# Optimization experiments

Hardware: AMD Instinct MI355X
Metric: run time of the kernel (lower is better)

The kernel has to match this reference:

```python
import jax, jax.numpy as jnp
import numpy as np

B, H, N = 1024, 1024, 32  # batch, d_model, d_state//2 (conjugate-symmetric diag)

def setup_inputs() -> dict:
    key = jax.random.key(0)
    ks = jax.random.split(key, 12)
    return {
        "u": jax.random.normal(ks[0], (B, H), jnp.float32),
        "state_re": jax.random.normal(ks[1], (B, H, N), jnp.float32),
        "state_im": jax.random.normal(ks[2], (B, H, N), jnp.float32),
        "dA_re": jax.random.normal(ks[3], (H, N), jnp.float32) * 0.3,
        "dA_im": jax.random.normal(ks[4], (H, N), jnp.float32) * 0.3,
        "dB_re": jax.random.normal(ks[5], (H, N), jnp.float32),
        "dB_im": jax.random.normal(ks[6], (H, N), jnp.float32),
        "C_re": jax.random.normal(ks[7], (H, N), jnp.float32),
        "C_im": jax.random.normal(ks[8], (H, N), jnp.float32),
        "D": jax.random.normal(ks[9], (H,), jnp.float32),
        "W": jax.random.normal(ks[10], (2 * H, H), jnp.float32) / np.sqrt(H),
        "b": jax.random.normal(ks[11], (2 * H,), jnp.float32) * 0.01,
    }

def reference(u, state_re, state_im, dA_re, dA_im, dB_re, dB_im, C_re, C_im, D, W, b):
    # Complex diagonal state update: next_state = dA * state + dB * u   [B,H,N]
    ue = u[..., None]
    ns_re = dA_re * state_re - dA_im * state_im + dB_re * ue
    ns_im = dA_re * state_im + dA_im * state_re + dB_im * ue
    # Readout: y = 2 * Re(sum_n C * next_state)   [B,H]  (channels=1)
    y = 2.0 * (jnp.einsum('hn,bhn->bh', C_re, ns_re)
               - jnp.einsum('hn,bhn->bh', C_im, ns_im))
    # Skip connection + exact GELU (torch default)
    y = jax.nn.gelu(y + u * D, approximate=False)
    # output_linear: Linear(H -> 2H) then GLU
    z = y @ W.T + b                      # [B, 2H]
    h = D.shape[0]
    y_out = z[:, :h] * jax.nn.sigmoid(z[:, h:])
    return y_out, ns_re, ns_im
```

## Files before the change

kernel.cpp:

```cpp
#include <hip/hip_runtime.h>
#include <math.h>

#define BB 1024
#define HH 1024
#define NN 32

typedef float f4 __attribute__((ext_vector_type(4)));

__global__ __launch_bounds__(256) void s4_update_kernel(
    const float* __restrict__ u,
    const float* __restrict__ sre,  const float* __restrict__ sim,
    const float* __restrict__ dAre, const float* __restrict__ dAim,
    const float* __restrict__ dBre, const float* __restrict__ dBim,
    const float* __restrict__ Cre,  const float* __restrict__ Cim,
    const float* __restrict__ Dv,
    float* __restrict__ nsre, float* __restrict__ nsim,
    float* __restrict__ Y)
{
    const int tid  = threadIdx.x;
    const long gid = (long)blockIdx.x * 256 + tid;
    const int pair = (int)(gid >> 3);
    const int sub  = tid & 7;
    const int n0   = sub << 2;
    const int h    = pair & (HH - 1);
    const size_t sbase = (size_t)pair * NN + n0;
    const int    pbase = h * NN + n0;

    const f4 a_re = *(const f4*)(dAre + pbase);
    const f4 a_im = *(const f4*)(dAim + pbase);
    const f4 b_re = *(const f4*)(dBre + pbase);
    const f4 b_im = *(const f4*)(dBim + pbase);
    const f4 c_re = *(const f4*)(Cre  + pbase);
    const f4 c_im = *(const f4*)(Cim  + pbase);
    const f4 s_re = *(const f4*)(sre + sbase);
    const f4 s_im = *(const f4*)(sim + sbase);
    const float uv = u[pair];

    f4 nre = a_re * s_re - a_im * s_im + b_re * uv;
    f4 nim = a_re * s_im + a_im * s_re + b_im * uv;

    *(f4*)(nsre + sbase) = nre;
    *(f4*)(nsim + sbase) = nim;

    f4 p = c_re * nre - c_im * nim;
    float part = p[0] + p[1] + p[2] + p[3];
    part += __shfl_xor(part, 1, 64);
    part += __shfl_xor(part, 2, 64);
    part += __shfl_xor(part, 4, 64);

    if (sub == 0) {
        float yv = 2.0f * part + uv * Dv[h];
        float g = 0.5f * yv * (1.0f + erff(yv * 0.70710678118654752f));
        Y[pair] = g;
    }
}

__global__ __launch_bounds__(256) void s4_gemm_glu_kernel(
    const float* __restrict__ Y, const float* __restrict__ W,
    const float* __restrict__ bias, float* __restrict__ out)
{
    __shared__ float Ys [16][68];
    __shared__ float W1s[16][68];
    __shared__ float W2s[16][68];

    const int tid  = threadIdx.x;
    const int row0 = blockIdx.y * 64;
    const int jc0  = blockIdx.x * 64;

    const int lr = tid >> 2;
    const int lk = (tid & 3) << 2;

    const float* Yg  = Y + (size_t)(row0 + lr) * HH + lk;
    const float* W1g = W + (size_t)(jc0 + lr) * HH + lk;
    const float* W2g = W + (size_t)(jc0 + 1024 + lr) * HH + lk;

    const int tc = tid & 15;
    const int tr = tid >> 4;

    float acc1[4][4] = {{0.f}};
    float acc2[4][4] = {{0.f}};

    for (int k0 = 0; k0 < HH; k0 += 16) {
        const f4 yv = *(const f4*)(Yg  + k0);
        const f4 w1 = *(const f4*)(W1g + k0);
        const f4 w2 = *(const f4*)(W2g + k0);

        __syncthreads();
        #pragma unroll
        for (int i = 0; i < 4; ++i) {
            Ys [lk + i][lr] = yv[i];
            W1s[lk + i][lr] = w1[i];
            W2s[lk + i][lr] = w2[i];
        }
        __syncthreads();

        #pragma unroll
        for (int kk = 0; kk < 16; ++kk) {
            const f4 ya  = *(const f4*)&Ys [kk][tr << 2];
            const f4 wa1 = *(const f4*)&W1s[kk][tc << 2];
            const f4 wa2 = *(const f4*)&W2s[kk][tc << 2];
            #pragma unroll
            for (int i = 0; i < 4; ++i) {
                #pragma unroll
                for (int j = 0; j < 4; ++j) {
                    acc1[i][j] = fmaf(ya[i], wa1[j], acc1[i][j]);
                    acc2[i][j] = fmaf(ya[i], wa2[j], acc2[i][j]);
                }
            }
        }
    }

    float b1[4], b2[4];
    #pragma unroll
    for (int j = 0; j < 4; ++j) {
        b1[j] = bias[jc0 + (tc << 2) + j];
        b2[j] = bias[jc0 + 1024 + (tc << 2) + j];
    }
    #pragma unroll
    for (int i = 0; i < 4; ++i) {
        f4 o;
        #pragma unroll
        for (int j = 0; j < 4; ++j) {
            float z1 = acc1[i][j] + b1[j];
            float z2 = acc2[i][j] + b2[j];
            o[j] = z1 * (1.0f / (1.0f + expf(-z2)));
        }
        *(f4*)(out + (size_t)(row0 + (tr << 2) + i) * HH + jc0 + (tc << 2)) = o;
    }
}

extern "C" void kernel_launch(void* const* d_in, const int* in_sizes, int n_in,
                              void* d_out, int out_size, void* d_ws, size_t ws_size,
                              hipStream_t stream) {
    const float* u    = (const float*)d_in[0];
    const float* sre  = (const float*)d_in[1];
    const float* sim  = (const float*)d_in[2];
    const float* dAre = (const float*)d_in[3];
    const float* dAim = (const float*)d_in[4];
    const float* dBre = (const float*)d_in[5];
    const float* dBim = (const float*)d_in[6];
    const float* Cre  = (const float*)d_in[7];
    const float* Cim  = (const float*)d_in[8];
    const float* Dv   = (const float*)d_in[9];
    const float* W    = (const float*)d_in[10];
    const float* bias = (const float*)d_in[11];

    float* out   = (float*)d_out;
    float* y_out = out;
    float* nsre  = out + (size_t)BB * HH;
    float* nsim  = nsre + (size_t)BB * HH * NN;
    float* Yws   = (float*)d_ws;

    const long total_threads = (long)BB * HH * 8;
    s4_update_kernel<<<dim3((unsigned)(total_threads / 256)), 256, 0, stream>>>(
        u, sre, sim, dAre, dAim, dBre, dBim, Cre, Cim, Dv, nsre, nsim, Yws);

    s4_gemm_glu_kernel<<<dim3(16, 16), 256, 0, stream>>>(Yws, W, bias, y_out);
}
```

Before: 565.8 us.

## Replace FP32 SIMT GEMM with split-bf16 MFMA GEMM fused with GLU

Splits Y and W into high and low bf16 parts (the update kernel writes Y's parts, a new kernel converts W each call). The GEMM becomes a matrix-core kernel that runs three bf16 MFMA products (hi*hi, hi*lo, lo*hi) to approximate FP32 accuracy, with GLU in the epilogue. It trades scalar FMA work for matrix-core throughput but adds a W conversion pass, extra workspace traffic and loads straight from global memory without LDS staging.

```diff
diff --git a/kernel.cpp b/kernel.cpp
--- a/kernel.cpp
+++ b/kernel.cpp
@@ -5,7 +5,20 @@
 #define HH 1024
 #define NN 32
 
-typedef float f4 __attribute__((ext_vector_type(4)));
+typedef float f4     __attribute__((ext_vector_type(4)));
+typedef float f32x4  __attribute__((ext_vector_type(4)));
+typedef short bf16x8 __attribute__((ext_vector_type(8)));
+typedef short s4v    __attribute__((ext_vector_type(4)));
+
+static __device__ __forceinline__ short f2bf(float x) {
+    unsigned u = __builtin_bit_cast(unsigned, x);
+    u += 0x7fff + ((u >> 16) & 1);
+    return (short)(u >> 16);
+}
+static __device__ __forceinline__ float bf2f(short h) {
+    unsigned u = ((unsigned)(unsigned short)h) << 16;
+    return __builtin_bit_cast(float, u);
+}
 
 __global__ __launch_bounds__(256) void s4_update_kernel(
     const float* __restrict__ u,
@@ -15,7 +28,7 @@
     const float* __restrict__ Cre,  const float* __restrict__ Cim,
     const float* __restrict__ Dv,
     float* __restrict__ nsre, float* __restrict__ nsim,
-    float* __restrict__ Y)
+    short* __restrict__ Yhi, short* __restrict__ Ylo)
 {
     const int tid  = threadIdx.x;
     const long gid = (long)blockIdx.x * 256 + tid;
@@ -51,81 +64,98 @@
     if (sub == 0) {
         float yv = 2.0f * part + uv * Dv[h];
         float g = 0.5f * yv * (1.0f + erff(yv * 0.70710678118654752f));
-        Y[pair] = g;
+        short hi = f2bf(g);
+        Yhi[pair] = hi;
+        Ylo[pair] = f2bf(g - bf2f(hi));
     }
 }
 
-__global__ __launch_bounds__(256) void s4_gemm_glu_kernel(
-    const float* __restrict__ Y, const float* __restrict__ W,
+__global__ __launch_bounds__(256) void wsplit_kernel(
+    const float* __restrict__ W, short* __restrict__ Whi, short* __restrict__ Wlo)
+{
+    const size_t i = ((size_t)blockIdx.x * 256 + threadIdx.x) * 4;
+    const f4 w = *(const f4*)(W + i);
+    s4v hi, lo;
+    #pragma unroll
+    for (int j = 0; j < 4; ++j) {
+        hi[j] = f2bf(w[j]);
+        lo[j] = f2bf(w[j] - bf2f(hi[j]));
+    }
+    *(s4v*)(Whi + i) = hi;
+    *(s4v*)(Wlo + i) = lo;
+}
+
+__global__ __launch_bounds__(256) void gemm_mfma_glu_kernel(
+    const short* __restrict__ Yhi, const short* __restrict__ Ylo,
+    const short* __restrict__ Whi, const short* __restrict__ Wlo,
     const float* __restrict__ bias, float* __restrict__ out)
 {
-    __shared__ float Ys [16][68];
-    __shared__ float W1s[16][68];
-    __shared__ float W2s[16][68];
+    const int tid  = threadIdx.x;
+    const int lane = tid & 63;
+    const int w    = tid >> 6;
+    const int wr   = w >> 1;
+    const int wc   = w & 1;
+    const int l15  = lane & 15;
+    const int g    = lane >> 4;
 
-    const int tid  = threadIdx.x;
-    const int row0 = blockIdx.y * 64;
-    const int jc0  = blockIdx.x * 64;
+    const int r0 = blockIdx.y * 64 + wr * 32;
+    const int jc = blockIdx.x * 32 + wc * 16;
 
-    const int lr = tid >> 2;
-    const int lk = (tid & 3) << 2;
+    const size_t rowA0 = (size_t)(r0 + l15) * HH;
+    const size_t rowA1 = rowA0 + (size_t)16 * HH;
+    const size_t rowB1 = (size_t)(jc + l15) * HH;
+    const size_t rowB2 = (size_t)(HH + jc + l15) * HH;
+    const int koff = g * 8;
 
-    const float* Yg  = Y + (size_t)(row0 + lr) * HH + lk;
-    const float* W1g = W + (size_t)(jc0 + lr) * HH + lk;
-    const float* W2g = W + (size_t)(jc0 + 1024 + lr) * HH + lk;
+    const short* pAh0 = Yhi + rowA0 + koff;
+    const short* pAh1 = Yhi + rowA1 + koff;
+    const short* pAl0 = Ylo + rowA0 + koff;
+    const short* pAl1 = Ylo + rowA1 + koff;
+    const short* pBh1 = Whi + rowB1 + koff;
+    const short* pBh2 = Whi + rowB2 + koff;
+    const short* pBl1 = Wlo + rowB1 + koff;
+    const short* pBl2 = Wlo + rowB2 + koff;
 
-    const int tc = tid & 15;
-    const int tr = tid >> 4;
+    f32x4 acc[2][2] = {};
 
-    float acc1[4][4] = {{0.f}};
-    float acc2[4][4] = {{0.f}};
+    #pragma unroll 2
+    for (int k0 = 0; k0 < HH; k0 += 32) {
+        const bf16x8 ah0 = *(const bf16x8*)(pAh0 + k0);
+        const bf16x8 ah1 = *(const bf16x8*)(pAh1 + k0);
+        const bf16x8 al0 = *(const bf16x8*)(pAl0 + k0);
+        const bf16x8 al1 = *(const bf16x8*)(pAl1 + k0);
+        const bf16x8 bh1 = *(const bf16x8*)(pBh1 + k0);
+        const bf16x8 bh2 = *(const bf16x8*)(pBh2 + k0);
+        const bf16x8 bl1 = *(const bf16x8*)(pBl1 + k0);
+        const bf16x8 bl2 = *(const bf16x8*)(pBl2 + k0);
 
-    for (int k0 = 0; k0 < HH; k0 += 16) {
-        const f4 yv = *(const f4*)(Yg  + k0);
-        const f4 w1 = *(const f4*)(W1g + k0);
-        const f4 w2 = *(const f4*)(W2g + k0);
+        acc[0][0] = __builtin_amdgcn_mfma_f32_16x16x32_bf16(ah0, bh1, acc[0][0], 0, 0, 0);
+        acc[0][1] = __builtin_amdgcn_mfma_f32_16x16x32_bf16(ah0, bh2, acc[0][1], 0, 0, 0);
+        acc[1][0] = __builtin_amdgcn_mfma_f32_16x16x32_bf16(ah1, bh1, acc[1][0], 0, 0, 0);
+        acc[1][1] = __builtin_amdgcn_mfma_f32_16x16x32_bf16(ah1, bh2, acc[1][1], 0, 0, 0);
 
-        __syncthreads();
-        #pragma unroll
-        for (int i = 0; i < 4; ++i) {
-            Ys [lk + i][lr] = yv[i];
-            W1s[lk + i][lr] = w1[i];
-            W2s[lk + i][lr] = w2[i];
-        }
-        __syncthreads();
+        acc[0][0] = __builtin_amdgcn_mfma_f32_16x16x32_bf16(ah0, bl1, acc[0][0], 0, 0, 0);
+        acc[0][1] = __builtin_amdgcn_mfma_f32_16x16x32_bf16(ah0, bl2, acc[0][1], 0, 0, 0);
+        acc[1][0] = __builtin_amdgcn_mfma_f32_16x16x32_bf16(ah1, bl1, acc[1][0], 0, 0, 0);
+        acc[1][1] = __builtin_amdgcn_mfma_f32_16x16x32_bf16(ah1, bl2, acc[1][1], 0, 0, 0);
 
-        #pragma unroll
-        for (int kk = 0; kk < 16; ++kk) {
-            const f4 ya  = *(const f4*)&Ys [kk][tr << 2];
-            const f4 wa1 = *(const f4*)&W1s[kk][tc << 2];
-            const f4 wa2 = *(const f4*)&W2s[kk][tc << 2];
-            #pragma unroll
-            for (int i = 0; i < 4; ++i) {
-                #pragma unroll
-                for (int j = 0; j < 4; ++j) {
-                    acc1[i][j] = fmaf(ya[i], wa1[j], acc1[i][j]);
-                    acc2[i][j] = fmaf(ya[i], wa2[j], acc2[i][j]);
-                }
-            }
-        }
+        acc[0][0] = __builtin_amdgcn_mfma_f32_16x16x32_bf16(al0, bh1, acc[0][0], 0, 0, 0);
+        acc[0][1] = __builtin_amdgcn_mfma_f32_16x16x32_bf16(al0, bh2, acc[0][1], 0, 0, 0);
+        acc[1][0] = __builtin_amdgcn_mfma_f32_16x16x32_bf16(al1, bh1, acc[1][0], 0, 0, 0);
+        acc[1][1] = __builtin_amdgcn_mfma_f32_16x16x32_bf16(al1, bh2, acc[1][1], 0, 0, 0);
     }
 
-    float b1[4], b2[4];
+    const float b1 = bias[jc + l15];
+    const float b2 = bias[HH + jc + l15];
     #pragma unroll
-    for (int j = 0; j < 4; ++j) {
-        b1[j] = bias[jc0 + (tc << 2) + j];
-        b2[j] = bias[jc0 + 1024 + (tc << 2) + j];
-    }
-    #pragma unroll
-    for (int i = 0; i < 4; ++i) {
-        f4 o;
+    for (int fr = 0; fr < 2; ++fr) {
         #pragma unroll
-        for (int j = 0; j < 4; ++j) {
-            float z1 = acc1[i][j] + b1[j];
-            float z2 = acc2[i][j] + b2[j];
-            o[j] = z1 * (1.0f / (1.0f + expf(-z2)));
+        for (int r = 0; r < 4; ++r) {
+            const int row = r0 + 16 * fr + 4 * g + r;
+            const float z1 = acc[fr][0][r] + b1;
+            const float z2 = acc[fr][1][r] + b2;
+            out[(size_t)row * HH + jc + l15] = z1 * (1.0f / (1.0f + expf(-z2)));
         }
-        *(f4*)(out + (size_t)(row0 + (tr << 2) + i) * HH + jc0 + (tc << 2)) = o;
     }
 }
 
@@ -149,11 +179,18 @@
     float* y_out = out;
     float* nsre  = out + (size_t)BB * HH;
     float* nsim  = nsre + (size_t)BB * HH * NN;
-    float* Yws   = (float*)d_ws;
+
+    short* Yhi = (short*)d_ws;
+    short* Ylo = Yhi + (size_t)BB * HH;
+    short* Whi = Ylo + (size_t)BB * HH;
+    short* Wlo = Whi + (size_t)2 * HH * HH;
+
+    wsplit_kernel<<<dim3(2 * HH * HH / 1024), 256, 0, stream>>>(W, Whi, Wlo);
 
     const long total_threads = (long)BB * HH * 8;
     s4_update_kernel<<<dim3((unsigned)(total_threads / 256)), 256, 0, stream>>>(
-        u, sre, sim, dAre, dAim, dBre, dBim, Cre, Cim, Dv, nsre, nsim, Yws);
+        u, sre, sim, dAre, dAim, dBre, dBim, Cre, Cim, Dv, nsre, nsim, Yhi, Ylo);
 
-    s4_gemm_glu_kernel<<<dim3(16, 16), 256, 0, stream>>>(Yws, W, bias, y_out);
+    gemm_mfma_glu_kernel<<<dim3(32, 16), 256, 0, stream>>>(
+        Yhi, Ylo, Whi, Wlo, bias, y_out);
 }
```

Result: faster. 538.6 us (-4.8%).
